# Performance work log

Hardware: AMD Instinct MI355X
Metric: run time of the kernel (lower is better)

The kernel has to match this reference:

```python
import jax, jax.numpy as jnp
import numpy as np
from jax import lax

INPUT_DIMS = [300, 74, 35]
HIDDEN_DIMS = [256, 64, 64]
OUT_CELL = 64
OUT_DIM = 1
B, T = 512, 128


def setup_inputs() -> dict:
    key = jax.random.key(0)
    ks = iter(jax.random.split(key, 32))
    d = {}
    for m, D in enumerate(INPUT_DIMS):
        d[f"x{m}"] = jax.random.normal(next(ks), (B, T, D), dtype=jnp.float32)
    s = 0.02
    for m, (D, H) in enumerate(zip(INPUT_DIMS, HIDDEN_DIMS)):
        d[f"w_ih{m}"] = jax.random.normal(next(ks), (4 * H, D), dtype=jnp.float32) * s
        d[f"w_hh{m}"] = jax.random.normal(next(ks), (4 * H, H), dtype=jnp.float32) * s
        d[f"b_ih{m}"] = jnp.zeros((4 * H,), dtype=jnp.float32)
        d[f"b_hh{m}"] = jnp.zeros((4 * H,), dtype=jnp.float32)
    sum_h = sum(HIDDEN_DIMS)
    d["w1"] = jax.random.normal(next(ks), (OUT_CELL, sum_h), dtype=jnp.float32) * s
    d["b1"] = jnp.zeros((OUT_CELL,), dtype=jnp.float32)
    d["w2"] = jax.random.normal(next(ks), (OUT_DIM, OUT_CELL), dtype=jnp.float32) * s
    d["b2"] = jnp.zeros((OUT_DIM,), dtype=jnp.float32)
    return d


def _lstm_last_h(x, w_ih, w_hh, b_ih, b_hh):
    # x: [B, T, D] -> last hidden state [B, H], torch.nn.LSTMCell gate order i,f,g,o
    Bsz = x.shape[0]
    H = w_hh.shape[1]
    xg = jnp.einsum("btd,gd->tbg", x, w_ih) + b_ih + b_hh  # precompute input projections [T,B,4H]

    def step(carry, xg_t):
        h, c = carry
        gates = xg_t + h @ w_hh.T
        i, f, g, o = jnp.split(gates, 4, axis=-1)
        c = jax.nn.sigmoid(f) * c + jax.nn.sigmoid(i) * jnp.tanh(g)
        h = jax.nn.sigmoid(o) * jnp.tanh(c)
        return (h, c), None

    h0 = jnp.zeros((Bsz, H), dtype=x.dtype)
    (h, _), _ = lax.scan(step, (h0, h0), xg)
    return h


def reference(x0, x1, x2,
              w_ih0, w_hh0, b_ih0, b_hh0,
              w_ih1, w_hh1, b_ih1, b_hh1,
              w_ih2, w_hh2, b_ih2, b_hh2,
              w1, b1, w2, b2):
    h0 = _lstm_last_h(x0, w_ih0, w_hh0, b_ih0, b_hh0)
    h1 = _lstm_last_h(x1, w_ih1, w_hh1, b_ih1, b_hh1)
    h2 = _lstm_last_h(x2, w_ih2, w_hh2, b_ih2, b_hh2)
    last_h = jnp.concatenate([h0, h1, h2], axis=1)  # [B, sum_h]
    hid = jax.nn.relu(last_h @ w1.T + b1)  # dropout = identity in eval
    return hid @ w2.T + b2  # [B, OUT_DIM]
```

## Files before the change

kernel.cpp:

```cpp
#include <hip/hip_runtime.h>

typedef _Float16 h8 __attribute__((ext_vector_type(8)));
typedef _Float16 h4 __attribute__((ext_vector_type(4)));
typedef float f4 __attribute__((ext_vector_type(4)));
typedef unsigned int u32x4 __attribute__((ext_vector_type(4)));
typedef unsigned long long u64;
typedef unsigned int u32;

__device__ __forceinline__ float sigm(float x) { return 1.f / (1.f + __expf(-x)); }
__device__ __forceinline__ float tanhf_(float x) { return 1.f - 2.f / (1.f + __expf(2.f * x)); }

__global__ __launch_bounds__(256) void pack_all(
    const float* __restrict__ wih0, const float* __restrict__ whh0,
    const float* __restrict__ wih1, const float* __restrict__ whh1,
    const float* __restrict__ wih2, const float* __restrict__ whh2,
    const float* __restrict__ bih0, const float* __restrict__ bhh0,
    const float* __restrict__ bih1, const float* __restrict__ bhh1,
    const float* __restrict__ bih2, const float* __restrict__ bhh2,
    _Float16* __restrict__ wihp0, _Float16* __restrict__ whhp0,
    _Float16* __restrict__ wihp1, _Float16* __restrict__ whhp1,
    _Float16* __restrict__ wihp2, _Float16* __restrict__ whhp2,
    float* __restrict__ biasc)
{
    if (blockIdx.x >= 324) {
        int bi = (blockIdx.x - 324) * 256 + threadIdx.x;
        if (bi < 1024)      biasc[bi] = bih0[bi] + bhh0[bi];
        else if (bi < 1280) biasc[bi] = bih1[bi - 1024] + bhh1[bi - 1024];
        else if (bi < 1536) biasc[bi] = bih2[bi - 1280] + bhh2[bi - 1280];
        return;
    }
    int s = blockIdx.x * 256 + threadIdx.x;
    const float* src; _Float16* dst; int KC, D;
    if (s < 40960)      {            dst = wihp0; src = wih0; KC = 10; D = 300; }
    else if (s < 73728) { s -= 40960; dst = whhp0; src = whh0; KC = 8;  D = 256; }
    else if (s < 76800) { s -= 73728; dst = wihp1; src = wih1; KC = 3;  D = 74;  }
    else if (s < 78848) { s -= 76800; dst = whhp1; src = whh1; KC = 2;  D = 64;  }
    else if (s < 80896) { s -= 78848; dst = wihp2; src = wih2; KC = 2;  D = 35;  }
    else                { s -= 80896; dst = whhp2; src = whh2; KC = 2;  D = 64;  }
    int lane = s & 63;
    int kc = (s >> 6) % KC;
    int gt = (s >> 6) / KC;
    int g = gt * 16 + (lane & 15);
    int kb = kc * 32 + ((lane >> 4) << 3);
    h8 v;
#pragma unroll
    for (int i = 0; i < 8; i++) {
        int k = kb + i;
        v[i] = (_Float16)((k < D) ? src[(size_t)g * D + k] : 0.f);
    }
    *(h8*)&dst[(size_t)s * 8] = v;
}

template <int M>
__device__ __forceinline__ void xg_block(int tc, int bq, int t0,
    const float* __restrict__ x, const _Float16* __restrict__ wihp,
    const float* __restrict__ bias, _Float16* __restrict__ xgp, _Float16* axf)
{
    constexpr int D   = (M == 0) ? 300 : ((M == 1) ? 74 : 35);
    constexpr int KCX = (M == 0) ? 10 : ((M == 1) ? 3 : 2);
    const int t = t0 + tc;
    const int tid = threadIdx.x, w = tid >> 6, l = tid & 63, ccol = l & 15;
    const int r0 = bq * 64;

    for (int sI = tid; sI < 4 * KCX * 64; sI += 512) {
        int rt = sI / (KCX * 64);
        int kc = (sI >> 6) % KCX;
        int ll = sI & 63;
        int row = r0 + rt * 16 + (ll & 15);
        int kb = kc * 32 + ((ll >> 4) << 3);
        const float* bp = x + ((size_t)row * 128 + t) * D + kb;
        h8 v;
#pragma unroll
        for (int i = 0; i < 8; i++) v[i] = (_Float16)((kb + i < D) ? bp[i] : 0.f);
        *(h8*)&axf[sI * 8] = v;
    }
    __syncthreads();

    if (M == 0) {
        f4 acc[4][8];
#pragma unroll
        for (int g = 0; g < 8; g++) {
            int gt = (g >> 1) * 16 + 2 * w + (g & 1);
            float b = bias[gt * 16 + ccol];
#pragma unroll
            for (int rt = 0; rt < 4; rt++) acc[rt][g] = (f4){b, b, b, b};
        }
#pragma unroll
        for (int kc = 0; kc < KCX; kc++) {
            h8 a[4];
#pragma unroll
            for (int rt = 0; rt < 4; rt++) a[rt] = *(const h8*)&axf[((rt * KCX + kc) * 64 + l) * 8];
#pragma unroll
            for (int g = 0; g < 8; g++) {
                int gt = (g >> 1) * 16 + 2 * w + (g & 1);
                h8 b = *(const h8*)&wihp[((size_t)(gt * KCX + kc) * 64 + l) * 8];
#pragma unroll
                for (int rt = 0; rt < 4; rt++)
                    acc[rt][g] = __builtin_amdgcn_mfma_f32_16x16x32_f16(a[rt], b, acc[rt][g], 0, 0, 0);
            }
        }
#pragma unroll
        for (int rtw = 0; rtw < 4; rtw++) {
            int gr = bq * 2 + (rtw >> 1), rt = rtw & 1;
#pragma unroll
            for (int gi = 0; gi < 8; gi++) {
                int ga = gi >> 1;
                int e = 2 * w + (gi & 1);
                int s2 = e >> 2;
                int w2 = (e & 3) * 2 + rt;
                f4 a = acc[rtw][gi];
                h4 v;
#pragma unroll
                for (int q = 0; q < 4; q++) v[q] = (_Float16)a[q];
                size_t off = (size_t)tc * 524288 +
                             ((((size_t)gr * 4 + s2) * 8 + w2) * 64 + l) * 16 + ga * 4;
                *(h4*)&xgp[off] = v;
            }
        }
    } else {
        const int rh = w >> 2, ht = w & 3;
        f4 acc[2][4];
#pragma unroll
        for (int ga = 0; ga < 4; ga++) {
            int gt = ga * 4 + ht;
            float b = bias[gt * 16 + ccol];
            acc[0][ga] = (f4){b, b, b, b};
            acc[1][ga] = (f4){b, b, b, b};
        }
#pragma unroll
        for (int kc = 0; kc < KCX; kc++) {
            h8 a[2];
#pragma unroll
            for (int rr = 0; rr < 2; rr++)
                a[rr] = *(const h8*)&axf[(((rh * 2 + rr) * KCX + kc) * 64 + l) * 8];
#pragma unroll
            for (int ga = 0; ga < 4; ga++) {
                int gt = ga * 4 + ht;
                h8 b = *(const h8*)&wihp[((size_t)(gt * KCX + kc) * 64 + l) * 8];
#pragma unroll
                for (int rr = 0; rr < 2; rr++)
                    acc[rr][ga] = __builtin_amdgcn_mfma_f32_16x16x32_f16(a[rr], b, acc[rr][ga], 0, 0, 0);
            }
        }
#pragma unroll
        for (int rr = 0; rr < 2; rr++)
#pragma unroll
        for (int gp = 0; gp < 2; gp++) {
            f4 lo = acc[rr][2 * gp], hi = acc[rr][2 * gp + 1];
            h8 v;
#pragma unroll
            for (int q = 0; q < 4; q++) { v[q] = (_Float16)lo[q]; v[4 + q] = (_Float16)hi[q]; }
            int fp = rr * 2 + gp;
            size_t off = ((((size_t)tc * 8 + bq) * 8 + w) * 4 + fp) * 64 + l;
            *(h8*)&xgp[off * 8] = v;
        }
    }
}

__global__ __launch_bounds__(512, 2) void xg_kernel(
    const float* __restrict__ x0, const float* __restrict__ x1, const float* __restrict__ x2,
    const _Float16* __restrict__ wihp0, const _Float16* __restrict__ wihp1,
    const _Float16* __restrict__ wihp2, const float* __restrict__ biasc,
    _Float16* __restrict__ xgp0, _Float16* __restrict__ xgp1, _Float16* __restrict__ xgp2,
    int t0, int TC)
{
    __shared__ __align__(16) _Float16 axf[4 * 10 * 64 * 8];
    int b = blockIdx.x;
    int per = TC * 8;
    if (b < per)            xg_block<0>(b >> 3, b & 7, t0, x0, wihp0, biasc,        xgp0, axf);
    else if (b < 2 * per) { b -= per;     xg_block<1>(b >> 3, b & 7, t0, x1, wihp1, biasc + 1024, xgp1, axf); }
    else                  { b -= 2 * per; xg_block<2>(b >> 3, b & 7, t0, x2, wihp2, biasc + 1280, xgp2, axf); }
}

__global__ __launch_bounds__(512, 1) void rec_kernel(
    const _Float16* __restrict__ whhp0, const _Float16* __restrict__ whhp1,
    const _Float16* __restrict__ whhp2,
    const _Float16* __restrict__ xgp0, const _Float16* __restrict__ xgp1,
    const _Float16* __restrict__ xgp2,
    float* __restrict__ h_all, float* __restrict__ csave, _Float16* __restrict__ hsave,
    u64* __restrict__ hx, u32* __restrict__ flags,
    int t0, int TC)
{
    __shared__ __align__(16) char smem[151552];
    const int bid = blockIdx.x;
    const int tid = threadIdx.x, w = tid >> 6, l = tid & 63;
    const int ccol = l & 15, crow = (l >> 4) * 4;

    if (bid < 64) {
        const int g = bid & 15, s = bid >> 4;
        const int r0 = g * 32;
        _Float16* whhs   = (_Float16*)smem;
        _Float16* apack  = (_Float16*)(smem + 131072);
        _Float16* hstage = (_Float16*)(smem + 147456);
        u64* apack_u64   = (u64*)apack;
        const int hgroup = w >> 1, rt = w & 1;
        const int s1 = (s + 1) & 3, s2 = (s + 2) & 3, s3 = (s + 3) & 3;

        for (int v = tid; v < 8192; v += 512) {
            int gtl = v >> 9, off = v & 511;
            int gt = (gtl >> 2) * 16 + s * 4 + (gtl & 3);
            ((u32x4*)whhs)[v] = ((const u32x4*)whhp0)[(size_t)gt * 512 + off];
        }
        float c[4];
        float* cs = csave + ((size_t)bid * 512 + tid) * 4;
        if (t0 == 0) {
#pragma unroll
            for (int i = 0; i < 4; i++) c[i] = 0.f;
            u32x4 z = (u32x4){0u, 0u, 0u, 0u};
            for (int v = tid; v < 1024; v += 512) ((u32x4*)apack)[v] = z;
        } else {
#pragma unroll
            for (int i = 0; i < 4; i++) c[i] = cs[i];
            for (int v = tid; v < 2048; v += 512)
                apack_u64[v] = __hip_atomic_load(&hx[((size_t)(t0 - 1) * 16 + g) * 2048 + v],
                                                 __ATOMIC_RELAXED, __HIP_MEMORY_SCOPE_AGENT);
        }
        __syncthreads();

        const _Float16* xgb = xgp0 + ((((size_t)g * 4 + s) * 8 + w) * 64 + l) * 16;
        h8 xcur0 = *(const h8*)&xgb[0];
        h8 xcur1 = *(const h8*)&xgb[8];

        f4 acc[4];
        for (int tc = 0; tc < TC; tc++) {
            const int t = t0 + tc;
#pragma unroll
            for (int q = 0; q < 4; q++) {
                acc[0][q] = (float)xcur0[q];
                acc[1][q] = (float)xcur0[4 + q];
                acc[2][q] = (float)xcur1[q];
                acc[3][q] = (float)xcur1[4 + q];
            }
            h8 xn0 = xcur0, xn1 = xcur1;
            if (tc + 1 < TC) {
                xn0 = *(const h8*)&xgb[(size_t)(tc + 1) * 524288];
                xn1 = *(const h8*)&xgb[(size_t)(tc + 1) * 524288 + 8];
            }
#pragma unroll
            for (int kc = 0; kc < 8; kc++) {
                h8 a = *(const h8*)&apack[((kc * 2 + rt) * 64 + l) * 8];
#pragma unroll
                for (int ga = 0; ga < 4; ga++) {
                    h8 b = *(const h8*)&whhs[(((ga * 4 + hgroup) * 8 + kc) * 64 + l) * 8];
                    acc[ga] = __builtin_amdgcn_mfma_f32_16x16x32_f16(a, b, acc[ga], 0, 0, 0);
                }
            }
#pragma unroll
            for (int q = 0; q < 4; q++) {
                float gi = acc[0][q], gf = acc[1][q], gg = acc[2][q], go = acc[3][q];
                float cn = sigm(gf) * c[q] + sigm(gi) * tanhf_(gg);
                c[q] = cn;
                float hv = sigm(go) * tanhf_(cn);
                int row = rt * 16 + crow + q;
                int hcol = hgroup * 16 + ccol;
                if (t == 127) {
                    h_all[(size_t)(r0 + row) * 384 + s * 64 + hcol] = hv;
                } else {
                    int lane2 = (((hcol & 31) >> 3) << 4) | (row & 15);
                    hstage[(((hcol >> 5) * 2 + rt) * 64 + lane2) * 8 + (l & 7)] = (_Float16)hv;
                }
            }
            xcur0 = xn0; xcur1 = xn1;
            __syncthreads();
            if (t < 127) {
                u64 hval = ((u64*)hstage)[tid];
                __hip_atomic_store(&hx[(((size_t)t * 16 + g) * 4 + s) * 512 + tid], hval,
                                   __ATOMIC_RELAXED, __HIP_MEMORY_SCOPE_AGENT);
                apack_u64[s * 512 + tid] = hval;
                __syncthreads();
                if (tid == 0)
                    __hip_atomic_store(&flags[((size_t)t * 16 + g) * 32 + s], 1u,
                                       __ATOMIC_RELAXED, __HIP_MEMORY_SCOPE_AGENT);
                const u32* fl = &flags[((size_t)t * 16 + g) * 32];
                while (true) {
                    u32 fa = __hip_atomic_load(&fl[s1], __ATOMIC_RELAXED, __HIP_MEMORY_SCOPE_AGENT);
                    u32 fb = __hip_atomic_load(&fl[s2], __ATOMIC_RELAXED, __HIP_MEMORY_SCOPE_AGENT);
                    u32 fc = __hip_atomic_load(&fl[s3], __ATOMIC_RELAXED, __HIP_MEMORY_SCOPE_AGENT);
                    if (fa + fb + fc == 3u) break;
                }
                const u64* hxs = &hx[(((size_t)t * 16 + g) * 4) * 512];
                u64 v1 = __hip_atomic_load(&hxs[s1 * 512 + tid], __ATOMIC_RELAXED, __HIP_MEMORY_SCOPE_AGENT);
                u64 v2 = __hip_atomic_load(&hxs[s2 * 512 + tid], __ATOMIC_RELAXED, __HIP_MEMORY_SCOPE_AGENT);
                u64 v3 = __hip_atomic_load(&hxs[s3 * 512 + tid], __ATOMIC_RELAXED, __HIP_MEMORY_SCOPE_AGENT);
                apack_u64[s1 * 512 + tid] = v1;
                apack_u64[s2 * 512 + tid] = v2;
                apack_u64[s3 * 512 + tid] = v3;
                __syncthreads();
            }
        }
        if (t0 + TC < 128) {
#pragma unroll
            for (int i = 0; i < 4; i++) cs[i] = c[i];
        }
    } else {
        const int m = (bid < 72) ? 1 : 2;
        const int lb = (bid - 64) & 7;
        const int r0 = lb * 64;
        const int colb = (m == 1) ? 256 : 320;
        const _Float16* whhp = (m == 1) ? whhp1 : whhp2;
        const _Float16* xgp  = (m == 1) ? xgp1 : xgp2;
        _Float16* whhs = (_Float16*)smem;
        _Float16* apkA = (_Float16*)(smem + 32768);
        _Float16* apkB = (_Float16*)(smem + 40960);
        const int rh = w >> 2, ht = w & 3;
        float c[8];
        h8 xbuf[4];
        float* cs = csave + 131072 + (((size_t)(bid - 64)) * 512 + tid) * 8;
        for (int v = tid; v < 2048; v += 512) ((u32x4*)whhs)[v] = ((const u32x4*)whhp)[v];
        if (t0 == 0) {
#pragma unroll
            for (int i = 0; i < 8; i++) c[i] = 0.f;
            u32x4 z = (u32x4){0u, 0u, 0u, 0u};
            for (int v = tid; v < 512; v += 512) ((u32x4*)apkA)[v] = z;
        } else {
#pragma unroll
            for (int i = 0; i < 8; i++) c[i] = cs[i];
            const u32x4* hsrc = (const u32x4*)(hsave + (size_t)(bid - 64) * 4096);
            for (int v = tid; v < 512; v += 512) ((u32x4*)apkA)[v] = hsrc[v];
        }
        __syncthreads();

        const size_t xbase = ((size_t)lb * 8 + w) * 4 * 512 + (size_t)l * 8;
#pragma unroll
        for (int fp = 0; fp < 4; fp++)
            xbuf[fp] = *(const h8*)&xgp[xbase + (size_t)fp * 512];

        f4 acc[2][4];
        for (int tc = 0; tc < TC; tc++) {
            _Float16* cur = (tc & 1) ? apkB : apkA;
            _Float16* nxt = (tc & 1) ? apkA : apkB;
#pragma unroll
            for (int rr = 0; rr < 2; rr++)
#pragma unroll
            for (int gp = 0; gp < 2; gp++) {
                int fp = rr * 2 + gp;
#pragma unroll
                for (int q = 0; q < 4; q++) {
                    acc[rr][2 * gp][q]     = (float)xbuf[fp][q];
                    acc[rr][2 * gp + 1][q] = (float)xbuf[fp][4 + q];
                }
            }
            if (tc + 1 < TC) {
                size_t nb = xbase + (size_t)(tc + 1) * 8 * 8 * 4 * 512;
#pragma unroll
                for (int fp = 0; fp < 4; fp++)
                    xbuf[fp] = *(const h8*)&xgp[nb + (size_t)fp * 512];
            }
#pragma unroll
            for (int kc = 0; kc < 2; kc++) {
                h8 a0 = *(const h8*)&cur[(((rh * 2 + 0) * 2 + kc) * 64 + l) * 8];
                h8 a1 = *(const h8*)&cur[(((rh * 2 + 1) * 2 + kc) * 64 + l) * 8];
#pragma unroll
                for (int ga = 0; ga < 4; ga++) {
                    int gt = ga * 4 + ht;
                    h8 b = *(const h8*)&whhs[((gt * 2 + kc) * 64 + l) * 8];
                    acc[0][ga] = __builtin_amdgcn_mfma_f32_16x16x32_f16(a0, b, acc[0][ga], 0, 0, 0);
                    acc[1][ga] = __builtin_amdgcn_mfma_f32_16x16x32_f16(a1, b, acc[1][ga], 0, 0, 0);
                }
            }
            const int t = t0 + tc;
#pragma unroll
            for (int rr = 0; rr < 2; rr++)
#pragma unroll
            for (int q = 0; q < 4; q++) {
                int idx = rr * 4 + q;
                float gi = acc[rr][0][q];
                float gf = acc[rr][1][q];
                float gg = acc[rr][2][q];
                float go = acc[rr][3][q];
                float cn = sigm(gf) * c[idx] + sigm(gi) * tanhf_(gg);
                c[idx] = cn;
                float hv = sigm(go) * tanhf_(cn);
                int row = (rh * 2 + rr) * 16 + crow + q;
                int hcol = ht * 16 + ccol;
                if (t == 127) h_all[(size_t)(r0 + row) * 384 + colb + hcol] = hv;
                int kch = ht >> 1;
                int sub = (ht & 1) * 2 + (ccol >> 3);
                nxt[(((row >> 4) * 2 + kch) * 64 + sub * 16 + (row & 15)) * 8 + (ccol & 7)] = (_Float16)hv;
            }
            __syncthreads();
        }
        if (t0 + TC < 128) {
#pragma unroll
            for (int i = 0; i < 8; i++) cs[i] = c[i];
            u32x4* hdst = (u32x4*)(hsave + (size_t)(bid - 64) * 4096);
            const u32x4* src = (const u32x4*)((TC & 1) ? apkB : apkA);
            for (int v = tid; v < 512; v += 512) hdst[v] = src[v];
        }
    }
}

__global__ __launch_bounds__(512) void mlp_kernel(const float* __restrict__ h_all,
                                                  const float* __restrict__ w1,
                                                  const float* __restrict__ b1,
                                                  const float* __restrict__ w2,
                                                  const float* __restrict__ b2,
                                                  float* __restrict__ out)
{
    __shared__ float w1s[64 * 385];
    __shared__ float hs[8 * 384];
    int tid = threadIdx.x;
    for (int idx = tid; idx < 64 * 384; idx += 512) {
        int j = idx / 384, k = idx - j * 384;
        w1s[j * 385 + k] = w1[idx];
    }
    int r0 = blockIdx.x * 8;
    for (int idx = tid; idx < 8 * 384; idx += 512) hs[idx] = h_all[(size_t)r0 * 384 + idx];
    __syncthreads();

    int w = tid >> 6, j = tid & 63;
    float accv = b1[j];
    const float* hrow = &hs[w * 384];
    for (int k = 0; k < 384; k++) accv = fmaf(hrow[k], w1s[j * 385 + k], accv);
    float hid = fmaxf(accv, 0.f);
    float v = hid * w2[j];
#pragma unroll
    for (int off = 32; off >= 1; off >>= 1) v += __shfl_xor(v, off, 64);
    if (j == 0) out[r0 + w] = v + b2[0];
}

extern "C" void kernel_launch(void* const* d_in, const int* in_sizes, int n_in,
                              void* d_out, int out_size, void* d_ws, size_t ws_size,
                              hipStream_t stream)
{
    const float* x0   = (const float*)d_in[0];
    const float* x1   = (const float*)d_in[1];
    const float* x2   = (const float*)d_in[2];
    const float* wih0 = (const float*)d_in[3];
    const float* whh0 = (const float*)d_in[4];
    const float* bih0 = (const float*)d_in[5];
    const float* bhh0 = (const float*)d_in[6];
    const float* wih1 = (const float*)d_in[7];
    const float* whh1 = (const float*)d_in[8];
    const float* bih1 = (const float*)d_in[9];
    const float* bhh1 = (const float*)d_in[10];
    const float* wih2 = (const float*)d_in[11];
    const float* whh2 = (const float*)d_in[12];
    const float* bih2 = (const float*)d_in[13];
    const float* bhh2 = (const float*)d_in[14];
    const float* w1   = (const float*)d_in[15];
    const float* b1   = (const float*)d_in[16];
    const float* w2   = (const float*)d_in[17];
    const float* b2   = (const float*)d_in[18];

    char* ws = (char*)d_ws;
    size_t off = 0;
    auto alloc = [&](size_t bytes) { size_t o = off; off = (off + bytes + 255) & ~255ULL; return o; };
    size_t o_wihp0 = alloc(655360);
    size_t o_whhp0 = alloc(524288);
    size_t o_wihp1 = alloc(49152);
    size_t o_whhp1 = alloc(32768);
    size_t o_wihp2 = alloc(32768);
    size_t o_whhp2 = alloc(32768);
    size_t o_bias  = alloc(6144);
    size_t o_hall  = alloc(786432);
    size_t o_csave = alloc(786432);
    size_t o_hsave = alloc(131072);
    size_t o_hx    = alloc(33554432);
    size_t o_flags = alloc(262144);
    size_t fixed = off;

    int TC = 128;
    while (TC > 1 && fixed + (size_t)TC * 1572864ULL + 1024 > ws_size) TC >>= 1;
    size_t o_xgp0 = alloc((size_t)TC * 1048576ULL);
    size_t o_xgp1 = alloc((size_t)TC * 262144ULL);
    size_t o_xgp2 = alloc((size_t)TC * 262144ULL);

    _Float16* wihp0 = (_Float16*)(ws + o_wihp0);
    _Float16* whhp0 = (_Float16*)(ws + o_whhp0);
    _Float16* wihp1 = (_Float16*)(ws + o_wihp1);
    _Float16* whhp1 = (_Float16*)(ws + o_whhp1);
    _Float16* wihp2 = (_Float16*)(ws + o_wihp2);
    _Float16* whhp2 = (_Float16*)(ws + o_whhp2);
    float*    biasc = (float*)(ws + o_bias);
    float*    hall  = (float*)(ws + o_hall);
    float*    csave = (float*)(ws + o_csave);
    _Float16* hsave = (_Float16*)(ws + o_hsave);
    u64*      hx    = (u64*)(ws + o_hx);
    u32*      flags = (u32*)(ws + o_flags);
    _Float16* xgp0  = (_Float16*)(ws + o_xgp0);
    _Float16* xgp1  = (_Float16*)(ws + o_xgp1);
    _Float16* xgp2  = (_Float16*)(ws + o_xgp2);

    hipMemsetAsync(ws + o_flags, 0, 262144, stream);

    pack_all<<<330, 256, 0, stream>>>(wih0, whh0, wih1, whh1, wih2, whh2,
                                      bih0, bhh0, bih1, bhh1, bih2, bhh2,
                                      wihp0, whhp0, wihp1, whhp1, wihp2, whhp2, biasc);

    for (int t0 = 0; t0 < 128; t0 += TC) {
        xg_kernel<<<24 * TC, 512, 0, stream>>>(x0, x1, x2, wihp0, wihp1, wihp2, biasc,
                                               xgp0, xgp1, xgp2, t0, TC);
        rec_kernel<<<80, 512, 0, stream>>>(whhp0, whhp1, whhp2, xgp0, xgp1, xgp2,
                                           hall, csave, hsave, hx, flags, t0, TC);
    }

    mlp_kernel<<<64, 512, 0, stream>>>(hall, w1, b1, w2, b2, (float*)d_out);
}
```

Baseline: 571.2 us.

## Replace per-block flags with per-wave release tags and drop a block barrier

The layer-0 recurrence now signals progress per wave with step-valued tags written with release ordering. Each wave waits only for the matching waves of its peer blocks, which removes a __syncthreads before the flag store and lets waves proceed independently. Spin loops now sleep briefly between polls. The xg kernel's shared buffer is enlarged and its occupancy hint is rewritten as waves_per_eu(2,2). This may lower LDS occupancy and adds more polling traffic per wave.

```diff
diff --git a/kernel.cpp b/kernel.cpp
--- a/kernel.cpp
+++ b/kernel.cpp
@@ -157,14 +157,15 @@
     }
 }
 
-__global__ __launch_bounds__(512, 2) void xg_kernel(
+__global__ __launch_bounds__(512) __attribute__((amdgpu_waves_per_eu(2, 2)))
+void xg_kernel(
     const float* __restrict__ x0, const float* __restrict__ x1, const float* __restrict__ x2,
     const _Float16* __restrict__ wihp0, const _Float16* __restrict__ wihp1,
     const _Float16* __restrict__ wihp2, const float* __restrict__ biasc,
     _Float16* __restrict__ xgp0, _Float16* __restrict__ xgp1, _Float16* __restrict__ xgp2,
     int t0, int TC)
 {
-    __shared__ __align__(16) _Float16 axf[4 * 10 * 64 * 8];
+    __shared__ __align__(16) _Float16 axf[49152];
     int b = blockIdx.x;
     int per = TC * 8;
     if (b < per)            xg_block<0>(b >> 3, b & 7, t0, x0, wihp0, biasc,        xgp0, axf);
@@ -178,7 +179,7 @@
     const _Float16* __restrict__ xgp0, const _Float16* __restrict__ xgp1,
     const _Float16* __restrict__ xgp2,
     float* __restrict__ h_all, float* __restrict__ csave, _Float16* __restrict__ hsave,
-    u64* __restrict__ hx, u32* __restrict__ flags,
+    u64* __restrict__ hx, u32* __restrict__ tags,
     int t0, int TC)
 {
     __shared__ __align__(16) char smem[151552];
@@ -194,7 +195,7 @@
         _Float16* hstage = (_Float16*)(smem + 147456);
         u64* apack_u64   = (u64*)apack;
         const int hgroup = w >> 1, rt = w & 1;
-        const int s1 = (s + 1) & 3, s2 = (s + 2) & 3, s3 = (s + 3) & 3;
+        const int sp1 = (s + 1) & 3, sp2 = (s + 2) & 3, sp3 = (s + 3) & 3;
 
         for (int v = tid; v < 8192; v += 512) {
             int gtl = v >> 9, off = v & 511;
@@ -211,9 +212,25 @@
         } else {
 #pragma unroll
             for (int i = 0; i < 4; i++) c[i] = cs[i];
-            for (int v = tid; v < 2048; v += 512)
-                apack_u64[v] = __hip_atomic_load(&hx[((size_t)(t0 - 1) * 16 + g) * 2048 + v],
-                                                 __ATOMIC_RELAXED, __HIP_MEMORY_SCOPE_AGENT);
+            const u32 tv = (u32)t0;
+            const u32* tg = &tags[((size_t)(t0 - 1) * 16 + g) * 32];
+            while (true) {
+                u32 a0 = __hip_atomic_load(&tg[s * 8 + w],   __ATOMIC_RELAXED, __HIP_MEMORY_SCOPE_AGENT);
+                u32 a1 = __hip_atomic_load(&tg[sp1 * 8 + w], __ATOMIC_RELAXED, __HIP_MEMORY_SCOPE_AGENT);
+                u32 a2 = __hip_atomic_load(&tg[sp2 * 8 + w], __ATOMIC_RELAXED, __HIP_MEMORY_SCOPE_AGENT);
+                u32 a3 = __hip_atomic_load(&tg[sp3 * 8 + w], __ATOMIC_RELAXED, __HIP_MEMORY_SCOPE_AGENT);
+                if (a0 == tv && a1 == tv && a2 == tv && a3 == tv) break;
+                __builtin_amdgcn_s_sleep(2);
+            }
+            const u64* hb = &hx[((size_t)(t0 - 1) * 16 + g) * 2048];
+            u64 d0 = __hip_atomic_load(&hb[s * 512 + tid],   __ATOMIC_RELAXED, __HIP_MEMORY_SCOPE_AGENT);
+            u64 d1 = __hip_atomic_load(&hb[sp1 * 512 + tid], __ATOMIC_RELAXED, __HIP_MEMORY_SCOPE_AGENT);
+            u64 d2 = __hip_atomic_load(&hb[sp2 * 512 + tid], __ATOMIC_RELAXED, __HIP_MEMORY_SCOPE_AGENT);
+            u64 d3 = __hip_atomic_load(&hb[sp3 * 512 + tid], __ATOMIC_RELAXED, __HIP_MEMORY_SCOPE_AGENT);
+            apack_u64[s * 512 + tid]   = d0;
+            apack_u64[sp1 * 512 + tid] = d1;
+            apack_u64[sp2 * 512 + tid] = d2;
+            apack_u64[sp3 * 512 + tid] = d3;
         }
         __syncthreads();
 
@@ -267,24 +284,25 @@
                 __hip_atomic_store(&hx[(((size_t)t * 16 + g) * 4 + s) * 512 + tid], hval,
                                    __ATOMIC_RELAXED, __HIP_MEMORY_SCOPE_AGENT);
                 apack_u64[s * 512 + tid] = hval;
-                __syncthreads();
-                if (tid == 0)
-                    __hip_atomic_store(&flags[((size_t)t * 16 + g) * 32 + s], 1u,
-                                       __ATOMIC_RELAXED, __HIP_MEMORY_SCOPE_AGENT);
-                const u32* fl = &flags[((size_t)t * 16 + g) * 32];
+                if (l == 0)
+                    __hip_atomic_store(&tags[(((size_t)t * 16 + g) * 4 + s) * 8 + w], (u32)(t + 1),
+                                       __ATOMIC_RELEASE, __HIP_MEMORY_SCOPE_AGENT);
+                const u32 tv = (u32)(t + 1);
+                const u32* tg = &tags[((size_t)t * 16 + g) * 32];
                 while (true) {
-                    u32 fa = __hip_atomic_load(&fl[s1], __ATOMIC_RELAXED, __HIP_MEMORY_SCOPE_AGENT);
-                    u32 fb = __hip_atomic_load(&fl[s2], __ATOMIC_RELAXED, __HIP_MEMORY_SCOPE_AGENT);
-                    u32 fc = __hip_atomic_load(&fl[s3], __ATOMIC_RELAXED, __HIP_MEMORY_SCOPE_AGENT);
-                    if (fa + fb + fc == 3u) break;
+                    u32 a1 = __hip_atomic_load(&tg[sp1 * 8 + w], __ATOMIC_RELAXED, __HIP_MEMORY_SCOPE_AGENT);
+                    u32 a2 = __hip_atomic_load(&tg[sp2 * 8 + w], __ATOMIC_RELAXED, __HIP_MEMORY_SCOPE_AGENT);
+                    u32 a3 = __hip_atomic_load(&tg[sp3 * 8 + w], __ATOMIC_RELAXED, __HIP_MEMORY_SCOPE_AGENT);
+                    if (a1 == tv && a2 == tv && a3 == tv) break;
+                    __builtin_amdgcn_s_sleep(2);
                 }
                 const u64* hxs = &hx[(((size_t)t * 16 + g) * 4) * 512];
-                u64 v1 = __hip_atomic_load(&hxs[s1 * 512 + tid], __ATOMIC_RELAXED, __HIP_MEMORY_SCOPE_AGENT);
-                u64 v2 = __hip_atomic_load(&hxs[s2 * 512 + tid], __ATOMIC_RELAXED, __HIP_MEMORY_SCOPE_AGENT);
-                u64 v3 = __hip_atomic_load(&hxs[s3 * 512 + tid], __ATOMIC_RELAXED, __HIP_MEMORY_SCOPE_AGENT);
-                apack_u64[s1 * 512 + tid] = v1;
-                apack_u64[s2 * 512 + tid] = v2;
-                apack_u64[s3 * 512 + tid] = v3;
+                u64 v1 = __hip_atomic_load(&hxs[sp1 * 512 + tid], __ATOMIC_RELAXED, __HIP_MEMORY_SCOPE_AGENT);
+                u64 v2 = __hip_atomic_load(&hxs[sp2 * 512 + tid], __ATOMIC_RELAXED, __HIP_MEMORY_SCOPE_AGENT);
+                u64 v3 = __hip_atomic_load(&hxs[sp3 * 512 + tid], __ATOMIC_RELAXED, __HIP_MEMORY_SCOPE_AGENT);
+                apack_u64[sp1 * 512 + tid] = v1;
+                apack_u64[sp2 * 512 + tid] = v2;
+                apack_u64[sp3 * 512 + tid] = v3;
                 __syncthreads();
             }
         }
@@ -457,7 +475,7 @@
     size_t o_csave = alloc(786432);
     size_t o_hsave = alloc(131072);
     size_t o_hx    = alloc(33554432);
-    size_t o_flags = alloc(262144);
+    size_t o_tags  = alloc(262144);
     size_t fixed = off;
 
     int TC = 128;
@@ -477,12 +495,12 @@
     float*    csave = (float*)(ws + o_csave);
     _Float16* hsave = (_Float16*)(ws + o_hsave);
     u64*      hx    = (u64*)(ws + o_hx);
-    u32*      flags = (u32*)(ws + o_flags);
+    u32*      tags  = (u32*)(ws + o_tags);
     _Float16* xgp0  = (_Float16*)(ws + o_xgp0);
     _Float16* xgp1  = (_Float16*)(ws + o_xgp1);
     _Float16* xgp2  = (_Float16*)(ws + o_xgp2);
 
-    hipMemsetAsync(ws + o_flags, 0, 262144, stream);
+    hipMemsetAsync(ws + o_tags, 0, 262144, stream);
 
     pack_all<<<330, 256, 0, stream>>>(wih0, whh0, wih1, whh1, wih2, whh2,
                                       bih0, bhh0, bih1, bhh1, bih2, bhh2,
@@ -492,7 +510,7 @@
         xg_kernel<<<24 * TC, 512, 0, stream>>>(x0, x1, x2, wihp0, wihp1, wihp2, biasc,
                                                xgp0, xgp1, xgp2, t0, TC);
         rec_kernel<<<80, 512, 0, stream>>>(whhp0, whhp1, whhp2, xgp0, xgp1, xgp2,
-                                           hall, csave, hsave, hx, flags, t0, TC);
+                                           hall, csave, hsave, hx, tags, t0, TC);
     }
 
     mlp_kernel<<<64, 512, 0, stream>>>(hall, w1, b1, w2, b2, (float*)d_out);
```

Measured after the change: 1.449 ms. 154% more time.
